# Kernel tuning notes

Hardware: AMD Instinct MI355X
Metric: run time of the kernel (lower is better)

The kernel has to match this reference:

```python
import jax, jax.numpy as jnp
import numpy as np

RATE = 0.1
INPUT_SHAPE = [8192]
BATCH_DIMS = 1
K = max(1, round(RATE * int(np.prod(INPUT_SHAPE))))  # 819


def setup_inputs() -> dict:
    key = jax.random.key(0)
    x = jax.random.normal(key, (4096, 8192), dtype=jnp.float32)
    return {"x": x}


def reference(x) -> jnp.ndarray:
    batch_flat = int(np.prod(x.shape[:BATCH_DIMS]))
    x_flat = x.reshape(batch_flat, -1)            # [B, D]
    ax = jnp.abs(x_flat)
    topk_vals, _ = jax.lax.top_k(ax, K)           # [B, K] sorted descending
    thr = topk_vals[:, -1:]                        # kth largest |x| per row
    mask = (ax >= thr).reshape(x.shape)
    return jnp.where(mask, x, jnp.zeros_like(x))
```

## Files before the change

kernel.cpp:

```cpp
#include <hip/hip_runtime.h>
#include <stdint.h>


constexpr int NCOLS = 8192;
constexpr int TPB   = 256;
constexpr int V4    = NCOLS / 4;
constexpr int VPT   = V4 / TPB;
constexpr int NH    = 257;

__global__ __launch_bounds__(TPB) void topk_row_kernel(const float* __restrict__ x,
                                                       float* __restrict__ out,
                                                       int K) {
  __shared__ uint32_t hist[4 * NH];
  __shared__ uint32_t sh_digit, sh_rem;

  const int row  = blockIdx.x;
  const int tid  = threadIdx.x;
  const int wave = tid >> 6;

  const uint4* xr = (const uint4*)(x) + (size_t)row * V4;

  uint4 v[VPT];
#pragma unroll
  for (int i = 0; i < VPT; ++i) v[i] = xr[tid + i * TPB];

  uint32_t prefix = 0, maskHi = 0, rem = (uint32_t)K;

  for (int pass = 0; pass < 4; ++pass) {
    const int shift = 24 - 8 * pass;

    for (int i = tid; i < 4 * NH; i += TPB) hist[i] = 0;
    __syncthreads();

    uint32_t* h = &hist[wave * NH];
#pragma unroll
    for (int i = 0; i < VPT; ++i) {
      uint32_t a0 = v[i].x & 0x7fffffffu;
      uint32_t a1 = v[i].y & 0x7fffffffu;
      uint32_t a2 = v[i].z & 0x7fffffffu;
      uint32_t a3 = v[i].w & 0x7fffffffu;
      if ((a0 & maskHi) == prefix) atomicAdd(&h[(a0 >> shift) & 255u], 1u);
      if ((a1 & maskHi) == prefix) atomicAdd(&h[(a1 >> shift) & 255u], 1u);
      if ((a2 & maskHi) == prefix) atomicAdd(&h[(a2 >> shift) & 255u], 1u);
      if ((a3 & maskHi) == prefix) atomicAdd(&h[(a3 >> shift) & 255u], 1u);
    }
    __syncthreads();

    uint32_t c = hist[tid] + hist[NH + tid] + hist[2 * NH + tid] + hist[3 * NH + tid];
    __syncthreads();
    hist[tid] = c;
    __syncthreads();
    for (int off = 1; off < 256; off <<= 1) {
      uint32_t add = (tid + off < 256) ? hist[tid + off] : 0u;
      __syncthreads();
      hist[tid] += add;
      __syncthreads();
    }
    uint32_t sD  = hist[tid];
    uint32_t sD1 = (tid < 255) ? hist[tid + 1] : 0u;
    if (sD >= rem && sD1 < rem) {
      sh_digit = (uint32_t)tid;
      sh_rem   = rem - sD1;
    }
    __syncthreads();
    prefix |= sh_digit << shift;
    maskHi |= 0xFFu << shift;
    rem = sh_rem;
    __syncthreads();
  }

  const uint32_t thr = prefix;
  uint4* outr = (uint4*)(out) + (size_t)row * V4;
#pragma unroll
  for (int i = 0; i < VPT; ++i) {
    uint4 o = v[i];
    o.x = ((o.x & 0x7fffffffu) >= thr) ? o.x : 0u;
    o.y = ((o.y & 0x7fffffffu) >= thr) ? o.y : 0u;
    o.z = ((o.z & 0x7fffffffu) >= thr) ? o.z : 0u;
    o.w = ((o.w & 0x7fffffffu) >= thr) ? o.w : 0u;
    outr[tid + i * TPB] = o;
  }
}

extern "C" void kernel_launch(void* const* d_in, const int* in_sizes, int n_in,
                              void* d_out, int out_size, void* d_ws, size_t ws_size,
                              hipStream_t stream) {
  (void)n_in; (void)out_size; (void)d_ws; (void)ws_size;
  const float* x = (const float*)d_in[0];
  float* out = (float*)d_out;
  const int rows = in_sizes[0] / NCOLS;
  const int K = (int)(0.1 * NCOLS + 0.5);
  topk_row_kernel<<<rows, TPB, 0, stream>>>(x, out, K);
}
```

Measured before the change: 265.3 us.

## Use three-pass 11/10/10-bit radix select with wave-shuffle suffix scan

Replaces the four 8-bit radix passes with three passes: 2048 bins over the top 11 bits, then two 1024-bin passes. It uses fewer per-wave histogram copies, zeroes shared memory with vector stores, and finds the digit with per-thread bin groups plus a wave-shuffle suffix scan instead of a barrier-heavy shared-memory scan. The goal is fewer passes over the registers and fewer __syncthreads. The trade-offs are more shared memory per block, which may lower occupancy, and more atomic contention on fewer histogram copies in the first pass.

```diff
diff --git a/kernel.cpp b/kernel.cpp
--- a/kernel.cpp
+++ b/kernel.cpp
@@ -6,70 +6,113 @@
 constexpr int TPB   = 256;
 constexpr int V4    = NCOLS / 4;
 constexpr int VPT   = V4 / TPB;
-constexpr int NH    = 257;
+
+constexpr int PAD = 8;
+constexpr int B1 = 2048, C1 = 2;
+constexpr int B2 = 1024, C2 = 4;
+constexpr int S1 = B1 + PAD;
+constexpr int S2 = B2 + PAD;
+constexpr int HW = (C2 * S2 > C1 * S1) ? C2 * S2 : C1 * S1;
+
+struct Shared {
+  uint32_t hist[HW];
+  uint32_t wavesum[4];
+  uint32_t digit;
+  uint32_t rem;
+};
+
+template <int BINS, int COPIES>
+__device__ __forceinline__ uint32_t run_phase(Shared& sh, const uint4 (&v)[VPT],
+                                              int dshift, int cshift, uint32_t cprefix,
+                                              uint32_t& rem, int tid, int lane, int wave) {
+  constexpr int BPT = BINS / TPB;
+  constexpr int STRIDE = BINS + PAD;
+  constexpr int ZW4 = (COPIES * STRIDE) / 4;
+
+  uint4* hz = (uint4*)sh.hist;
+  for (int i = tid; i < ZW4; i += TPB) hz[i] = make_uint4(0u, 0u, 0u, 0u);
+  __syncthreads();
+
+  uint32_t* h = &sh.hist[((wave * COPIES) >> 2) * STRIDE];
+#pragma unroll
+  for (int i = 0; i < VPT; ++i) {
+    uint32_t a[4] = {v[i].x, v[i].y, v[i].z, v[i].w};
+#pragma unroll
+    for (int j = 0; j < 4; ++j) {
+      uint32_t key = a[j] & 0x7fffffffu;
+      if ((key >> cshift) == cprefix)
+        atomicAdd(&h[(key >> dshift) & (BINS - 1)], 1u);
+    }
+  }
+  __syncthreads();
+
+  uint32_t hb[BPT];
+#pragma unroll
+  for (int j = 0; j < BPT; ++j) hb[j] = 0;
+#pragma unroll
+  for (int c = 0; c < COPIES; ++c) {
+    const uint4* hp = (const uint4*)&sh.hist[c * STRIDE + tid * BPT];
+#pragma unroll
+    for (int q = 0; q < BPT / 4; ++q) {
+      uint4 t = hp[q];
+      hb[4 * q + 0] += t.x; hb[4 * q + 1] += t.y;
+      hb[4 * q + 2] += t.z; hb[4 * q + 3] += t.w;
+    }
+  }
+  uint32_t L = 0;
+#pragma unroll
+  for (int j = 0; j < BPT; ++j) L += hb[j];
+
+  uint32_t suf = L;
+#pragma unroll
+  for (int off = 1; off < 64; off <<= 1) {
+    uint32_t o = __shfl_down(suf, off, 64);
+    suf += (lane + off < 64) ? o : 0u;
+  }
+  if (lane == 0) sh.wavesum[wave] = suf;
+  __syncthreads();
+  uint32_t addw = 0;
+#pragma unroll
+  for (int w = 0; w < 4; ++w) addw += (w > wave) ? sh.wavesum[w] : 0u;
+  suf += addw;
+
+  uint32_t s = suf - L;
+#pragma unroll
+  for (int j = BPT - 1; j >= 0; --j) {
+    uint32_t snext = s;
+    s += hb[j];
+    if (s >= rem && snext < rem) {
+      sh.digit = (uint32_t)(tid * BPT + j);
+      sh.rem = rem - snext;
+    }
+  }
+  __syncthreads();
+  uint32_t d = sh.digit;
+  rem = sh.rem;
+  return d;
+}
 
 __global__ __launch_bounds__(TPB) void topk_row_kernel(const float* __restrict__ x,
                                                        float* __restrict__ out,
                                                        int K) {
-  __shared__ uint32_t hist[4 * NH];
-  __shared__ uint32_t sh_digit, sh_rem;
-
+  __shared__ Shared sh;
   const int row  = blockIdx.x;
   const int tid  = threadIdx.x;
+  const int lane = tid & 63;
   const int wave = tid >> 6;
 
   const uint4* xr = (const uint4*)(x) + (size_t)row * V4;
-
   uint4 v[VPT];
 #pragma unroll
   for (int i = 0; i < VPT; ++i) v[i] = xr[tid + i * TPB];
 
-  uint32_t prefix = 0, maskHi = 0, rem = (uint32_t)K;
+  uint32_t rem = (uint32_t)K;
+  uint32_t d1 = run_phase<B1, C1>(sh, v, 20, 31, 0u, rem, tid, lane, wave);
+  uint32_t d2 = run_phase<B2, C2>(sh, v, 10, 20, d1, rem, tid, lane, wave);
+  uint32_t d3 = run_phase<B2, C2>(sh, v,  0, 10, (d1 << 10) | d2, rem, tid, lane, wave);
 
-  for (int pass = 0; pass < 4; ++pass) {
-    const int shift = 24 - 8 * pass;
+  const uint32_t thr = (d1 << 20) | (d2 << 10) | d3;
 
-    for (int i = tid; i < 4 * NH; i += TPB) hist[i] = 0;
-    __syncthreads();
-
-    uint32_t* h = &hist[wave * NH];
-#pragma unroll
-    for (int i = 0; i < VPT; ++i) {
-      uint32_t a0 = v[i].x & 0x7fffffffu;
-      uint32_t a1 = v[i].y & 0x7fffffffu;
-      uint32_t a2 = v[i].z & 0x7fffffffu;
-      uint32_t a3 = v[i].w & 0x7fffffffu;
-      if ((a0 & maskHi) == prefix) atomicAdd(&h[(a0 >> shift) & 255u], 1u);
-      if ((a1 & maskHi) == prefix) atomicAdd(&h[(a1 >> shift) & 255u], 1u);
-      if ((a2 & maskHi) == prefix) atomicAdd(&h[(a2 >> shift) & 255u], 1u);
-      if ((a3 & maskHi) == prefix) atomicAdd(&h[(a3 >> shift) & 255u], 1u);
-    }
-    __syncthreads();
-
-    uint32_t c = hist[tid] + hist[NH + tid] + hist[2 * NH + tid] + hist[3 * NH + tid];
-    __syncthreads();
-    hist[tid] = c;
-    __syncthreads();
-    for (int off = 1; off < 256; off <<= 1) {
-      uint32_t add = (tid + off < 256) ? hist[tid + off] : 0u;
-      __syncthreads();
-      hist[tid] += add;
-      __syncthreads();
-    }
-    uint32_t sD  = hist[tid];
-    uint32_t sD1 = (tid < 255) ? hist[tid + 1] : 0u;
-    if (sD >= rem && sD1 < rem) {
-      sh_digit = (uint32_t)tid;
-      sh_rem   = rem - sD1;
-    }
-    __syncthreads();
-    prefix |= sh_digit << shift;
-    maskHi |= 0xFFu << shift;
-    rem = sh_rem;
-    __syncthreads();
-  }
-
-  const uint32_t thr = prefix;
   uint4* outr = (uint4*)(out) + (size_t)row * V4;
 #pragma unroll
   for (int i = 0; i < VPT; ++i) {
```

After: 231.5 us. -12.8%, faster.

## Process one row per wave with 10-bit radix passes and no block barriers

Applied to the files above, without the earlier changes.

Each 64-lane wave now handles a whole row, keeping 128 uint4 values per lane in registers. The radix select runs three 10-bit passes on private per-wave LDS histograms, then resolves the last bit with a ballot and count. Prefix scans use wave shuffles instead of block-wide __syncthreads scans, which removes barrier and scan overhead. The cost is very high register pressure (512 floats per lane), which risks spills or low occupancy despite launch_bounds(256,3), and the grid shrinks to rows/4 blocks.

```diff
diff --git a/kernel.cpp b/kernel.cpp
--- a/kernel.cpp
+++ b/kernel.cpp
@@ -4,81 +4,113 @@
 
 constexpr int NCOLS = 8192;
 constexpr int TPB   = 256;
-constexpr int V4    = NCOLS / 4;
-constexpr int VPT   = V4 / TPB;
-constexpr int NH    = 257;
+constexpr int WAVES = TPB / 64;
+constexpr int V4R   = NCOLS / 4;
+constexpr int V4L   = V4R / 64;
+constexpr int BINS  = 1024;
 
-__global__ __launch_bounds__(TPB) void topk_row_kernel(const float* __restrict__ x,
-                                                       float* __restrict__ out,
-                                                       int K) {
-  __shared__ uint32_t hist[4 * NH];
-  __shared__ uint32_t sh_digit, sh_rem;
+__global__ __launch_bounds__(TPB, 3) void topk_row_kernel(const float* __restrict__ x,
+                                                          float* __restrict__ out,
+                                                          int K) {
+  __shared__ uint32_t hist_all[WAVES * BINS];
+  const int tid  = threadIdx.x;
+  const int lane = tid & 63;
+  const int wave = tid >> 6;
+  const int row  = blockIdx.x * WAVES + wave;
+  uint32_t* h = &hist_all[wave * BINS];
 
-  const int row  = blockIdx.x;
-  const int tid  = threadIdx.x;
-  const int wave = tid >> 6;
+  const uint4* xr = (const uint4*)(x) + (size_t)row * V4R;
+  uint4 v[V4L];
+#pragma unroll
+  for (int c = 0; c < V4L; ++c) v[c] = xr[c * 64 + lane];
 
-  const uint4* xr = (const uint4*)(x) + (size_t)row * V4;
+  uint32_t rem = (uint32_t)K;
+  uint32_t pfx = 0;
 
-  uint4 v[VPT];
+#pragma unroll 1
+  for (int phase = 0; phase < 3; ++phase) {
+    const int dshift = 21 - 10 * phase;
+
 #pragma unroll
-  for (int i = 0; i < VPT; ++i) v[i] = xr[tid + i * TPB];
+    for (int t = 0; t < BINS / 64; ++t) h[t * 64 + lane] = 0u;
 
-  uint32_t prefix = 0, maskHi = 0, rem = (uint32_t)K;
+    if (phase == 0) {
+#pragma unroll
+      for (int c = 0; c < V4L; ++c) {
+        atomicAdd(&h[(v[c].x & 0x7fffffffu) >> 21], 1u);
+        atomicAdd(&h[(v[c].y & 0x7fffffffu) >> 21], 1u);
+        atomicAdd(&h[(v[c].z & 0x7fffffffu) >> 21], 1u);
+        atomicAdd(&h[(v[c].w & 0x7fffffffu) >> 21], 1u);
+      }
+    } else {
+      const int cshift = dshift + 10;
+#pragma unroll
+      for (int c = 0; c < V4L; ++c) {
+        uint32_t k;
+        k = v[c].x & 0x7fffffffu; if ((k >> cshift) == pfx) atomicAdd(&h[(k >> dshift) & (BINS - 1)], 1u);
+        k = v[c].y & 0x7fffffffu; if ((k >> cshift) == pfx) atomicAdd(&h[(k >> dshift) & (BINS - 1)], 1u);
+        k = v[c].z & 0x7fffffffu; if ((k >> cshift) == pfx) atomicAdd(&h[(k >> dshift) & (BINS - 1)], 1u);
+        k = v[c].w & 0x7fffffffu; if ((k >> cshift) == pfx) atomicAdd(&h[(k >> dshift) & (BINS - 1)], 1u);
+      }
+    }
 
-  for (int pass = 0; pass < 4; ++pass) {
-    const int shift = 24 - 8 * pass;
+    uint32_t Tl = 0;
+#pragma unroll
+    for (int t = 0; t < 16; ++t) Tl += h[lane * 16 + ((t + lane) & 15)];
 
-    for (int i = tid; i < 4 * NH; i += TPB) hist[i] = 0;
-    __syncthreads();
+    uint32_t S = Tl;
+#pragma unroll
+    for (int off = 1; off < 64; off <<= 1) {
+      uint32_t u = __shfl_down(S, off, 64);
+      S += (lane + off < 64) ? u : 0u;
+    }
+    uint32_t Sx = S - Tl;
+    uint64_t bal = __ballot(S >= rem && Sx < rem);
+    int W = __ffsll((unsigned long long)bal) - 1;
+    uint32_t SxW = __shfl(Sx, W, 64);
 
-    uint32_t* h = &hist[wave * NH];
+    uint32_t cv = h[W * 16 + (lane & 15)];
+    uint32_t s2 = cv;
 #pragma unroll
-    for (int i = 0; i < VPT; ++i) {
-      uint32_t a0 = v[i].x & 0x7fffffffu;
-      uint32_t a1 = v[i].y & 0x7fffffffu;
-      uint32_t a2 = v[i].z & 0x7fffffffu;
-      uint32_t a3 = v[i].w & 0x7fffffffu;
-      if ((a0 & maskHi) == prefix) atomicAdd(&h[(a0 >> shift) & 255u], 1u);
-      if ((a1 & maskHi) == prefix) atomicAdd(&h[(a1 >> shift) & 255u], 1u);
-      if ((a2 & maskHi) == prefix) atomicAdd(&h[(a2 >> shift) & 255u], 1u);
-      if ((a3 & maskHi) == prefix) atomicAdd(&h[(a3 >> shift) & 255u], 1u);
+    for (int off = 1; off < 16; off <<= 1) {
+      uint32_t u = __shfl_down(s2, off, 64);
+      s2 += (((lane & 15) + off) < 16) ? u : 0u;
     }
-    __syncthreads();
-
-    uint32_t c = hist[tid] + hist[NH + tid] + hist[2 * NH + tid] + hist[3 * NH + tid];
-    __syncthreads();
-    hist[tid] = c;
-    __syncthreads();
-    for (int off = 1; off < 256; off <<= 1) {
-      uint32_t add = (tid + off < 256) ? hist[tid + off] : 0u;
-      __syncthreads();
-      hist[tid] += add;
-      __syncthreads();
-    }
-    uint32_t sD  = hist[tid];
-    uint32_t sD1 = (tid < 255) ? hist[tid + 1] : 0u;
-    if (sD >= rem && sD1 < rem) {
-      sh_digit = (uint32_t)tid;
-      sh_rem   = rem - sD1;
-    }
-    __syncthreads();
-    prefix |= sh_digit << shift;
-    maskHi |= 0xFFu << shift;
-    rem = sh_rem;
-    __syncthreads();
+    uint32_t s2x = s2 - cv;
+    uint64_t bal2 = __ballot((SxW + s2) >= rem && (SxW + s2x) < rem);
+    int LF = __ffsll((unsigned long long)bal2) - 1;
+    uint32_t digit = (uint32_t)(W * 16 + (LF & 15));
+    uint32_t SbinP1 = __shfl(SxW + s2x, LF, 64);
+    rem -= SbinP1;
+    pfx = (pfx << 10) | digit;
   }
 
-  const uint32_t thr = prefix;
-  uint4* outr = (uint4*)(out) + (size_t)row * V4;
+  uint32_t c1 = 0;
 #pragma unroll
-  for (int i = 0; i < VPT; ++i) {
-    uint4 o = v[i];
+  for (int c = 0; c < V4L; ++c) {
+    uint32_t k;
+    k = v[c].x & 0x7fffffffu; c1 += (uint32_t)((k >> 1) == pfx) & (k & 1u);
+    k = v[c].y & 0x7fffffffu; c1 += (uint32_t)((k >> 1) == pfx) & (k & 1u);
+    k = v[c].z & 0x7fffffffu; c1 += (uint32_t)((k >> 1) == pfx) & (k & 1u);
+    k = v[c].w & 0x7fffffffu; c1 += (uint32_t)((k >> 1) == pfx) & (k & 1u);
+  }
+#pragma unroll
+  for (int off = 1; off < 64; off <<= 1) {
+    uint32_t u = __shfl_down(c1, off, 64);
+    c1 += (lane + off < 64) ? u : 0u;
+  }
+  uint32_t c1tot = __shfl(c1, 0, 64);
+  const uint32_t thr = (pfx << 1) | ((c1tot >= rem) ? 1u : 0u);
+
+  uint4* outr = (uint4*)(out) + (size_t)row * V4R;
+#pragma unroll
+  for (int c = 0; c < V4L; ++c) {
+    uint4 o = v[c];
     o.x = ((o.x & 0x7fffffffu) >= thr) ? o.x : 0u;
     o.y = ((o.y & 0x7fffffffu) >= thr) ? o.y : 0u;
     o.z = ((o.z & 0x7fffffffu) >= thr) ? o.z : 0u;
     o.w = ((o.w & 0x7fffffffu) >= thr) ? o.w : 0u;
-    outr[tid + i * TPB] = o;
+    outr[c * 64 + lane] = o;
   }
 }
 
@@ -90,5 +122,5 @@
   float* out = (float*)d_out;
   const int rows = in_sizes[0] / NCOLS;
   const int K = (int)(0.1 * NCOLS + 0.5);
-  topk_row_kernel<<<rows, TPB, 0, stream>>>(x, out, K);
+  topk_row_kernel<<<rows / WAVES, TPB, 0, stream>>>(x, out, K);
 }
```

New measurement: 378.8 us. 1.43x slower.
